# Kernel tuning notes

Hardware: AMD Instinct MI355X
Metric: run time of the kernel (lower is better)

Reference implementation:

```python
import jax, jax.numpy as jnp
import numpy as np

B, S, E, H = 4, 2048, 1024, 16
D = E // H  # head dim = 64

def setup_inputs() -> dict:
    key = jax.random.key(0)
    k1, k2, k3 = jax.random.split(key, 3)
    scale = 0.02
    return {
        "x": jax.random.normal(k1, (B, S, E), dtype=jnp.float32),
        "W_qkv": jax.random.normal(k2, (E, 3 * E), dtype=jnp.float32) * scale,
        "b_qkv": jnp.zeros((3 * E,), dtype=jnp.float32),
        "W_o": jax.random.normal(k3, (E, E), dtype=jnp.float32) * scale,
        "b_o": jnp.zeros((E,), dtype=jnp.float32),
    }

def reference(x, W_qkv, b_qkv, W_o, b_o):
    # dropout is identity in eval mode
    qkv = x @ W_qkv + b_qkv                      # [B, S, 3E]
    q, k, v = jnp.split(qkv, 3, axis=-1)          # each [B, S, E]
    def split_heads(t):
        return t.reshape(B, S, H, D).transpose(0, 2, 1, 3)  # [B, H, S, D]
    q, k, v = split_heads(q), split_heads(k), split_heads(v)
    scores = jnp.einsum("bhsd,bhtd->bhst", q, k) / jnp.sqrt(jnp.float32(D))
    causal = jnp.tril(jnp.ones((S, S), dtype=bool))
    scores = jnp.where(causal[None, None], scores, jnp.float32(-jnp.inf))
    attn = jax.nn.softmax(scores, axis=-1)        # [B, H, S, S]
    out = jnp.einsum("bhst,bhtd->bhsd", attn, v)  # [B, H, S, D]
    out = out.transpose(0, 2, 1, 3).reshape(B, S, E)
    return out @ W_o + b_o
```

## Files before the change

### kernel.cpp

```cpp
#include <hip/hip_runtime.h>
#include <stdint.h>

typedef __bf16 bf16_t;
typedef __bf16 bf16x8 __attribute__((ext_vector_type(8)));
typedef float f32x4 __attribute__((ext_vector_type(4)));

#define LOG2E 1.44269504088896340736f

__device__ __forceinline__ float fexp2(float x) {
#if __has_builtin(__builtin_amdgcn_exp2f)
    return __builtin_amdgcn_exp2f(x);
#else
    return exp2f(x);
#endif
}

__device__ __forceinline__ void gld_lds16(const bf16_t* g, bf16_t* l) {
    __builtin_amdgcn_global_load_lds(
        (__attribute__((address_space(1))) void*)(bf16_t*)g,
        (__attribute__((address_space(3))) void*)l,
        16, 0, 0);
}

__global__ __launch_bounds__(256) void prep_k(
    const float* __restrict__ x, bf16_t* __restrict__ xb,
    const float* __restrict__ Wqkv, bf16_t* __restrict__ wqkvT,
    const float* __restrict__ Wo, bf16_t* __restrict__ woT)
{
    __shared__ float t[32][33];
    const int tid = threadIdx.x;
    int blk = blockIdx.x;
    if (blk < 8192) {
        int i = blk * 1024 + tid * 4;
        float4 v = *(const float4*)(x + i);
        union { bf16_t b[4]; uint2 u; } u;
        u.b[0] = (bf16_t)v.x; u.b[1] = (bf16_t)v.y; u.b[2] = (bf16_t)v.z; u.b[3] = (bf16_t)v.w;
        *(uint2*)(xb + i) = u.u;
        return;
    }
    const float* in; bf16_t* out; int C, bx, by;
    if (blk < 11264) { blk -= 8192; in = Wqkv; out = wqkvT; C = 3072; bx = blk % 96; by = blk / 96; }
    else             { blk -= 11264; in = Wo;   out = woT;   C = 1024; bx = blk % 32; by = blk / 32; }
    const int R = 1024;
    const int tx = tid & 31, ty = tid >> 5;
    const int c0 = bx * 32, r0 = by * 32;
    #pragma unroll
    for (int j = 0; j < 32; j += 8)
        t[ty + j][tx] = in[(size_t)(r0 + ty + j) * C + c0 + tx];
    __syncthreads();
    #pragma unroll
    for (int j = 0; j < 32; j += 8)
        out[(size_t)(c0 + ty + j) * R + r0 + tx] = (bf16_t)t[tx][ty + j];
}

__device__ __forceinline__ void gemm_body_3deep(
    const bf16_t* __restrict__ A, const bf16_t* __restrict__ Bt,
    bf16_t* Al, bf16_t* Bl, f32x4 (&acc)[4][4], int m0, int n0)
{
    const int tid = threadIdx.x;
    const int w = tid >> 6, lane = tid & 63;
    const int l15 = lane & 15, quad = lane >> 4;
    const int wm = w >> 1, wn = w & 1;

    const int srow = lane >> 3;
    const int scg = ((lane & 7) ^ srow) * 8;
    const bf16_t* Ag = A  + (size_t)(m0 + w * 32 + srow) * 1024 + scg;
    const bf16_t* Bg = Bt + (size_t)(n0 + w * 16 + srow) * 1024 + scg;
    bf16_t* Ald = Al + (w * 32) * 64;
    bf16_t* Bld = Bl + (w * 16) * 64;

    const int rc0 = (quad ^ (l15 & 7)) * 8;
    const int rc1 = ((quad + 4) ^ (l15 & 7)) * 8;

    auto stage = [&](int t, int s) {
        const int koff = t * 64;
        #pragma unroll
        for (int j = 0; j < 4; j++)
            gld_lds16(Ag + koff + (size_t)(j * 8) * 1024,
                      Ald + s * 16384 + (j * 8) * 64);
        #pragma unroll
        for (int j = 0; j < 2; j++)
            gld_lds16(Bg + koff + (size_t)(j * 8) * 1024,
                      Bld + s * 8192 + (j * 8) * 64);
    };

    stage(0, 0);
    stage(1, 1);
    asm volatile("s_waitcnt vmcnt(6)" ::: "memory");
    __builtin_amdgcn_s_barrier();

    int cur = 0, stg = 2;
    for (int t = 0; t < 16; ++t) {
        if (t < 14) stage(t + 2, stg);
        const bf16_t* Ab = Al + cur * 16384;
        const bf16_t* Bb = Bl + cur * 8192;
        #pragma unroll
        for (int hh = 0; hh < 2; hh++) {
            const int rc = hh ? rc1 : rc0;
            bf16x8 af[4], bfr[4];
            #pragma unroll
            for (int mi = 0; mi < 4; mi++)
                af[mi] = *(const bf16x8*)(Ab + (wm * 64 + mi * 16 + l15) * 64 + rc);
            #pragma unroll
            for (int ni = 0; ni < 4; ni++)
                bfr[ni] = *(const bf16x8*)(Bb + (wn * 64 + ni * 16 + l15) * 64 + rc);
            __builtin_amdgcn_s_setprio(1);
            #pragma unroll
            for (int mi = 0; mi < 4; mi++)
                #pragma unroll
                for (int ni = 0; ni < 4; ni++)
                    acc[mi][ni] = __builtin_amdgcn_mfma_f32_16x16x32_bf16(
                        af[mi], bfr[ni], acc[mi][ni], 0, 0, 0);
            __builtin_amdgcn_s_setprio(0);
        }
        if (t < 15) {
            if (t < 14) asm volatile("s_waitcnt vmcnt(6)" ::: "memory");
            else        asm volatile("s_waitcnt vmcnt(0)" ::: "memory");
            __builtin_amdgcn_s_barrier();
        }
        cur = (cur == 2) ? 0 : cur + 1;
        stg = (stg == 2) ? 0 : stg + 1;
    }
}

__global__ __launch_bounds__(512) void gemm_qkv_k(
    const bf16_t* __restrict__ X, const bf16_t* __restrict__ WT,
    const float* __restrict__ bias,
    bf16_t* __restrict__ Qb, bf16_t* __restrict__ Kb, bf16_t* __restrict__ VTb)
{
    __shared__ bf16_t Al[3 * 256 * 64];
    __shared__ bf16_t Bl[3 * 128 * 64];
    const int tid = threadIdx.x;
    const int lane = tid & 63, w = tid >> 6;
    const int l15 = lane & 15, quad = lane >> 4;
    const int wm = w >> 1, wn = w & 1;
    const int n0 = blockIdx.x * 128;
    const int m0 = blockIdx.y * 256;

    f32x4 acc[4][4];
    #pragma unroll
    for (int mi = 0; mi < 4; mi++)
        #pragma unroll
        for (int ni = 0; ni < 4; ni++) acc[mi][ni] = (f32x4){0.f, 0.f, 0.f, 0.f};

    gemm_body_3deep(WT, X, Al, Bl, acc, m0, n0);

    const float QSCALE = 0.125f * LOG2E;
    const int region = m0 >> 10;
    #pragma unroll
    for (int mi = 0; mi < 4; mi++) {
        const int mbase = m0 + wm * 64 + mi * 16 + quad * 4;
        const float4 bia = *(const float4*)(bias + mbase);
        const float ba[4] = {bia.x, bia.y, bia.z, bia.w};
        const int col = mbase & 1023;
        const int h = col >> 6, dbase = col & 63;
        #pragma unroll
        for (int ni = 0; ni < 4; ni++) {
            const int n = n0 + wn * 64 + ni * 16 + l15;
            const int b = n >> 11, s = n & 2047;
            if (region == 0) {
                union { bf16_t bv[4]; uint2 u; } u;
                #pragma unroll
                for (int r = 0; r < 4; r++)
                    u.bv[r] = (bf16_t)((acc[mi][ni][r] + ba[r]) * QSCALE);
                *(uint2*)(Qb + (((size_t)b * 16 + h) * 2048 + s) * 64 + dbase) = u.u;
            } else if (region == 1) {
                union { bf16_t bv[4]; uint2 u; } u;
                #pragma unroll
                for (int r = 0; r < 4; r++)
                    u.bv[r] = (bf16_t)(acc[mi][ni][r] + ba[r]);
                *(uint2*)(Kb + (((size_t)b * 16 + h) * 2048 + s) * 64 + dbase) = u.u;
            } else {
                bf16_t* dst = VTb + (((size_t)b * 16 + h) * 64 + dbase) * 2048 + s;
                #pragma unroll
                for (int r = 0; r < 4; r++)
                    dst[(size_t)r * 2048] = (bf16_t)(acc[mi][ni][r] + ba[r]);
            }
        }
    }
}

__global__ __launch_bounds__(256) void attn_k(
    const bf16_t* __restrict__ Qb, const bf16_t* __restrict__ Kb,
    const bf16_t* __restrict__ VTb, bf16_t* __restrict__ Ob)
{
    __shared__ bf16_t Kl[64 * 64];
    __shared__ bf16_t Vl[64 * 64];
    __shared__ bf16_t Pl[4][16 * 72];

    const int tid = threadIdx.x;
    const int w = tid >> 6, lane = tid & 63;
    const int l15 = lane & 15, quad = lane >> 4;
    const int idx = blockIdx.x;
    const int qt = 31 - (idx >> 6);
    const int bh = idx & 63;
    const int b = bh >> 4, h = bh & 15;
    const int q0 = qt * 64;

    const bf16_t* Qp = Qb + (size_t)bh * 2048 * 64;
    const bf16_t* Kp = Kb + (size_t)bh * 2048 * 64;
    const bf16_t* Vp = VTb + (size_t)bh * 64 * 2048;

    const int srow = w * 16 + (lane >> 3);
    const int scol = ((lane & 7) ^ ((lane >> 3) & 7)) * 8;
    const int rc0 = (quad ^ (l15 & 7)) * 8;
    const int rc1 = ((quad + 4) ^ (l15 & 7)) * 8;

    const int qrow = q0 + w * 16 + l15;
    bf16x8 aq0 = *(const bf16x8*)(Qp + (size_t)qrow * 64 + quad * 8);
    bf16x8 aq1 = *(const bf16x8*)(Qp + (size_t)qrow * 64 + 32 + quad * 8);

    bf16x8 vone;
    #pragma unroll
    for (int j = 0; j < 8; j++) vone[j] = (bf16_t)1.0f;

    f32x4 o[4];
    #pragma unroll
    for (int ni = 0; ni < 4; ni++) o[ni] = (f32x4){0.f, 0.f, 0.f, 0.f};
    f32x4 lacc = (f32x4){0.f, 0.f, 0.f, 0.f};
    const int qloc = w * 16 + l15;

    for (int kv0 = 0; kv0 <= q0; kv0 += 64) {
        __syncthreads();
        gld_lds16(Kp + (size_t)(kv0 + srow) * 64 + scol, Kl + (w * 16) * 64);
        gld_lds16(Kp + (size_t)(kv0 + srow + 8) * 64 + scol, Kl + (w * 16 + 8) * 64);
        gld_lds16(Vp + (size_t)srow * 2048 + kv0 + scol, Vl + (w * 16) * 64);
        gld_lds16(Vp + (size_t)(srow + 8) * 2048 + kv0 + scol, Vl + (w * 16 + 8) * 64);
        __syncthreads();

        f32x4 sv[4];
        #pragma unroll
        for (int ni = 0; ni < 4; ni++) {
            bf16x8 ak0 = *(const bf16x8*)(Kl + (ni * 16 + l15) * 64 + rc0);
            bf16x8 ak1 = *(const bf16x8*)(Kl + (ni * 16 + l15) * 64 + rc1);
            f32x4 z = (f32x4){0.f, 0.f, 0.f, 0.f};
            z = __builtin_amdgcn_mfma_f32_16x16x32_bf16(ak0, aq0, z, 0, 0, 0);
            z = __builtin_amdgcn_mfma_f32_16x16x32_bf16(ak1, aq1, z, 0, 0, 0);
            sv[ni] = z;
        }

        if (kv0 == q0) {
            #pragma unroll
            for (int ni = 0; ni < 4; ni++)
                #pragma unroll
                for (int r = 0; r < 4; r++)
                    if (ni * 16 + quad * 4 + r > qloc) sv[ni][r] = -INFINITY;
        }

        #pragma unroll
        for (int ni = 0; ni < 4; ni++) {
            union { bf16_t bv[4]; uint2 u; } pk;
            #pragma unroll
            for (int r = 0; r < 4; r++) pk.bv[r] = (bf16_t)fexp2(sv[ni][r]);
            *(uint2*)(&Pl[w][l15 * 72 + ni * 16 + quad * 4]) = pk.u;
        }

        bf16x8 pa0 = *(const bf16x8*)(&Pl[w][l15 * 72 + quad * 8]);
        bf16x8 pa1 = *(const bf16x8*)(&Pl[w][l15 * 72 + 32 + quad * 8]);
        #pragma unroll
        for (int ni = 0; ni < 4; ni++) {
            bf16x8 bv0 = *(const bf16x8*)(Vl + (ni * 16 + l15) * 64 + rc0);
            bf16x8 bv1 = *(const bf16x8*)(Vl + (ni * 16 + l15) * 64 + rc1);
            o[ni] = __builtin_amdgcn_mfma_f32_16x16x32_bf16(bv0, pa0, o[ni], 0, 0, 0);
            o[ni] = __builtin_amdgcn_mfma_f32_16x16x32_bf16(bv1, pa1, o[ni], 0, 0, 0);
        }
        lacc = __builtin_amdgcn_mfma_f32_16x16x32_bf16(vone, pa0, lacc, 0, 0, 0);
        lacc = __builtin_amdgcn_mfma_f32_16x16x32_bf16(vone, pa1, lacc, 0, 0, 0);
    }

    const float inv = 1.0f / lacc[0];
    const int s = q0 + w * 16 + l15;
    bf16_t* obase = Ob + ((size_t)b * 2048 + s) * 1024 + h * 64;
    #pragma unroll
    for (int ni = 0; ni < 4; ni++) {
        union { bf16_t bv[4]; uint2 u; } u;
        #pragma unroll
        for (int r = 0; r < 4; r++) u.bv[r] = (bf16_t)(o[ni][r] * inv);
        *(uint2*)(obase + ni * 16 + quad * 4) = u.u;
    }
}

__global__ __launch_bounds__(512) void gemm_out_k(
    const bf16_t* __restrict__ O, const bf16_t* __restrict__ WT,
    const float* __restrict__ bias, float* __restrict__ out)
{
    __shared__ bf16_t Al[3 * 256 * 64];
    __shared__ bf16_t Bl[3 * 128 * 64];
    const int tid = threadIdx.x;
    const int lane = tid & 63, w = tid >> 6;
    const int l15 = lane & 15, quad = lane >> 4;
    const int wm = w >> 1, wn = w & 1;
    const int n0 = blockIdx.x * 128;
    const int m0 = blockIdx.y * 256;

    f32x4 acc[4][4];
    #pragma unroll
    for (int mi = 0; mi < 4; mi++)
        #pragma unroll
        for (int ni = 0; ni < 4; ni++) acc[mi][ni] = (f32x4){0.f, 0.f, 0.f, 0.f};

    gemm_body_3deep(WT, O, Al, Bl, acc, m0, n0);

    #pragma unroll
    for (int mi = 0; mi < 4; mi++) {
        const int mbase = m0 + wm * 64 + mi * 16 + quad * 4;
        const float4 bia = *(const float4*)(bias + mbase);
        #pragma unroll
        for (int ni = 0; ni < 4; ni++) {
            const int n = n0 + wn * 64 + ni * 16 + l15;
            float4 v;
            v.x = acc[mi][ni][0] + bia.x;
            v.y = acc[mi][ni][1] + bia.y;
            v.z = acc[mi][ni][2] + bia.z;
            v.w = acc[mi][ni][3] + bia.w;
            *(float4*)(out + (size_t)n * 1024 + mbase) = v;
        }
    }
}


extern "C" void kernel_launch(void* const* d_in, const int* in_sizes, int n_in,
                              void* d_out, int out_size, void* d_ws, size_t ws_size,
                              hipStream_t stream) {
    const float* x     = (const float*)d_in[0];
    const float* W_qkv = (const float*)d_in[1];
    const float* b_qkv = (const float*)d_in[2];
    const float* W_o   = (const float*)d_in[3];
    const float* b_o   = (const float*)d_in[4];
    float* out = (float*)d_out;

    char* ws = (char*)d_ws;
    size_t off = 0;
    auto alloc = [&](size_t bytes) -> void* {
        void* p = ws + off;
        off += (bytes + 255) & ~(size_t)255;
        return p;
    };
    bf16_t* xb    = (bf16_t*)alloc((size_t)8192 * 1024 * 2);
    bf16_t* wqkvT = (bf16_t*)alloc((size_t)3072 * 1024 * 2);
    bf16_t* woT   = (bf16_t*)alloc((size_t)1024 * 1024 * 2);
    bf16_t* Qb    = (bf16_t*)alloc((size_t)8192 * 1024 * 2);
    bf16_t* Kb    = (bf16_t*)alloc((size_t)8192 * 1024 * 2);
    bf16_t* VTb   = (bf16_t*)alloc((size_t)8192 * 1024 * 2);
    bf16_t* Ob    = xb;

    prep_k<<<12288, 256, 0, stream>>>(x, xb, W_qkv, wqkvT, W_o, woT);
    gemm_qkv_k<<<dim3(64, 12), 512, 0, stream>>>(xb, wqkvT, b_qkv, Qb, Kb, VTb);
    attn_k<<<2048, 256, 0, stream>>>(Qb, Kb, VTb, Ob);
    gemm_out_k<<<dim3(64, 4), 512, 0, stream>>>(Ob, woT, b_o, out);
}
```

Measured before the change: 255.3 us.

## Retile GEMMs to 128x256 and split global-to-LDS loads across k-halves

Both projection GEMMs flip their block tile from 256(M)x128(N) to 128(M)x256(N), with waves arranged 2x4 instead of 4x2, and the launch grids change to match. The main loop now splits each 64-wide k-tile into two halves. Each half issues part of the next-next tile's global-to-LDS loads after its LDS fragment reads, then uses barriers to separate reads from MFMAs. The aim is to spread memory traffic more evenly and overlap it with MFMA work, at the cost of four barriers per k-tile instead of one.

Measured after the change: 237.4 us. 7.0% less time.

```diff
diff --git a/kernel.cpp b/kernel.cpp
--- a/kernel.cpp
+++ b/kernel.cpp
@@ -53,57 +53,54 @@
         out[(size_t)(c0 + ty + j) * R + r0 + tx] = (bf16_t)t[tx][ty + j];
 }
 
-__device__ __forceinline__ void gemm_body_3deep(
+__device__ __forceinline__ void gemm_body_pipe(
     const bf16_t* __restrict__ A, const bf16_t* __restrict__ Bt,
     bf16_t* Al, bf16_t* Bl, f32x4 (&acc)[4][4], int m0, int n0)
 {
     const int tid = threadIdx.x;
     const int w = tid >> 6, lane = tid & 63;
     const int l15 = lane & 15, quad = lane >> 4;
-    const int wm = w >> 1, wn = w & 1;
+    const int wm = w >> 2, wn = w & 3;
 
     const int srow = lane >> 3;
     const int scg = ((lane & 7) ^ srow) * 8;
-    const bf16_t* Ag = A  + (size_t)(m0 + w * 32 + srow) * 1024 + scg;
-    const bf16_t* Bg = Bt + (size_t)(n0 + w * 16 + srow) * 1024 + scg;
-    bf16_t* Ald = Al + (w * 32) * 64;
-    bf16_t* Bld = Bl + (w * 16) * 64;
+    const bf16_t* Ag = A  + (size_t)(m0 + w * 16 + srow) * 1024 + scg;
+    const bf16_t* Bg = Bt + (size_t)(n0 + w * 32 + srow) * 1024 + scg;
 
     const int rc0 = (quad ^ (l15 & 7)) * 8;
     const int rc1 = ((quad + 4) ^ (l15 & 7)) * 8;
 
-    auto stage = [&](int t, int s) {
-        const int koff = t * 64;
-        #pragma unroll
-        for (int j = 0; j < 4; j++)
-            gld_lds16(Ag + koff + (size_t)(j * 8) * 1024,
-                      Ald + s * 16384 + (j * 8) * 64);
-        #pragma unroll
-        for (int j = 0; j < 2; j++)
-            gld_lds16(Bg + koff + (size_t)(j * 8) * 1024,
-                      Bld + s * 8192 + (j * 8) * 64);
+    auto stage0 = [&](int kt, int ss) {
+        gld_lds16(Ag + kt * 64,                       Al + ss * 8192  + (w * 16) * 64);
+        gld_lds16(Ag + kt * 64 + (size_t)8 * 1024,    Al + ss * 8192  + (w * 16 + 8) * 64);
+        gld_lds16(Bg + kt * 64,                       Bl + ss * 16384 + (w * 32) * 64);
     };
-
-    stage(0, 0);
-    stage(1, 1);
+    auto stage1 = [&](int kt, int ss) {
+        gld_lds16(Bg + kt * 64 + (size_t)8 * 1024,    Bl + ss * 16384 + (w * 32 + 8) * 64);
+        gld_lds16(Bg + kt * 64 + (size_t)16 * 1024,   Bl + ss * 16384 + (w * 32 + 16) * 64);
+        gld_lds16(Bg + kt * 64 + (size_t)24 * 1024,   Bl + ss * 16384 + (w * 32 + 24) * 64);
+    };
+
+    stage0(0, 0); stage1(0, 0);
+    stage0(1, 1); stage1(1, 1);
     asm volatile("s_waitcnt vmcnt(6)" ::: "memory");
     __builtin_amdgcn_s_barrier();
 
-    int cur = 0, stg = 2;
+    int cs = 0, ss = 2;
     for (int t = 0; t < 16; ++t) {
-        if (t < 14) stage(t + 2, stg);
-        const bf16_t* Ab = Al + cur * 16384;
-        const bf16_t* Bb = Bl + cur * 8192;
-        #pragma unroll
-        for (int hh = 0; hh < 2; hh++) {
-            const int rc = hh ? rc1 : rc0;
+        const bf16_t* Ab = Al + cs * 8192;
+        const bf16_t* Bb = Bl + cs * 16384;
+
+        {
             bf16x8 af[4], bfr[4];
             #pragma unroll
             for (int mi = 0; mi < 4; mi++)
-                af[mi] = *(const bf16x8*)(Ab + (wm * 64 + mi * 16 + l15) * 64 + rc);
+                af[mi] = *(const bf16x8*)(Ab + (wm * 64 + mi * 16 + l15) * 64 + rc0);
             #pragma unroll
             for (int ni = 0; ni < 4; ni++)
-                bfr[ni] = *(const bf16x8*)(Bb + (wn * 64 + ni * 16 + l15) * 64 + rc);
+                bfr[ni] = *(const bf16x8*)(Bb + (wn * 64 + ni * 16 + l15) * 64 + rc0);
+            if (t < 14) stage0(t + 2, ss);
+            __builtin_amdgcn_s_barrier();
             __builtin_amdgcn_s_setprio(1);
             #pragma unroll
             for (int mi = 0; mi < 4; mi++)
@@ -112,14 +109,37 @@
                     acc[mi][ni] = __builtin_amdgcn_mfma_f32_16x16x32_bf16(
                         af[mi], bfr[ni], acc[mi][ni], 0, 0, 0);
             __builtin_amdgcn_s_setprio(0);
-        }
-        if (t < 15) {
-            if (t < 14) asm volatile("s_waitcnt vmcnt(6)" ::: "memory");
-            else        asm volatile("s_waitcnt vmcnt(0)" ::: "memory");
             __builtin_amdgcn_s_barrier();
         }
-        cur = (cur == 2) ? 0 : cur + 1;
-        stg = (stg == 2) ? 0 : stg + 1;
+
+        {
+            bf16x8 af[4], bfr[4];
+            #pragma unroll
+            for (int mi = 0; mi < 4; mi++)
+                af[mi] = *(const bf16x8*)(Ab + (wm * 64 + mi * 16 + l15) * 64 + rc1);
+            #pragma unroll
+            for (int ni = 0; ni < 4; ni++)
+                bfr[ni] = *(const bf16x8*)(Bb + (wn * 64 + ni * 16 + l15) * 64 + rc1);
+            if (t < 14) {
+                stage1(t + 2, ss);
+                asm volatile("s_waitcnt vmcnt(6)" ::: "memory");
+            } else if (t == 14) {
+                asm volatile("s_waitcnt vmcnt(0)" ::: "memory");
+            }
+            __builtin_amdgcn_s_barrier();
+            __builtin_amdgcn_s_setprio(1);
+            #pragma unroll
+            for (int mi = 0; mi < 4; mi++)
+                #pragma unroll
+                for (int ni = 0; ni < 4; ni++)
+                    acc[mi][ni] = __builtin_amdgcn_mfma_f32_16x16x32_bf16(
+                        af[mi], bfr[ni], acc[mi][ni], 0, 0, 0);
+            __builtin_amdgcn_s_setprio(0);
+            __builtin_amdgcn_s_barrier();
+        }
+
+        cs = (cs == 2) ? 0 : cs + 1;
+        ss = (ss == 2) ? 0 : ss + 1;
     }
 }
 
@@ -128,14 +148,14 @@
     const float* __restrict__ bias,
     bf16_t* __restrict__ Qb, bf16_t* __restrict__ Kb, bf16_t* __restrict__ VTb)
 {
-    __shared__ bf16_t Al[3 * 256 * 64];
-    __shared__ bf16_t Bl[3 * 128 * 64];
+    __shared__ bf16_t Al[3 * 128 * 64];
+    __shared__ bf16_t Bl[3 * 256 * 64];
     const int tid = threadIdx.x;
     const int lane = tid & 63, w = tid >> 6;
     const int l15 = lane & 15, quad = lane >> 4;
-    const int wm = w >> 1, wn = w & 1;
-    const int n0 = blockIdx.x * 128;
-    const int m0 = blockIdx.y * 256;
+    const int wm = w >> 2, wn = w & 3;
+    const int n0 = blockIdx.x * 256;
+    const int m0 = blockIdx.y * 128;
 
     f32x4 acc[4][4];
     #pragma unroll
@@ -143,7 +163,7 @@
         #pragma unroll
         for (int ni = 0; ni < 4; ni++) acc[mi][ni] = (f32x4){0.f, 0.f, 0.f, 0.f};
 
-    gemm_body_3deep(WT, X, Al, Bl, acc, m0, n0);
+    gemm_body_pipe(WT, X, Al, Bl, acc, m0, n0);
 
     const float QSCALE = 0.125f * LOG2E;
     const int region = m0 >> 10;
@@ -284,14 +304,14 @@
     const bf16_t* __restrict__ O, const bf16_t* __restrict__ WT,
     const float* __restrict__ bias, float* __restrict__ out)
 {
-    __shared__ bf16_t Al[3 * 256 * 64];
-    __shared__ bf16_t Bl[3 * 128 * 64];
+    __shared__ bf16_t Al[3 * 128 * 64];
+    __shared__ bf16_t Bl[3 * 256 * 64];
     const int tid = threadIdx.x;
     const int lane = tid & 63, w = tid >> 6;
     const int l15 = lane & 15, quad = lane >> 4;
-    const int wm = w >> 1, wn = w & 1;
-    const int n0 = blockIdx.x * 128;
-    const int m0 = blockIdx.y * 256;
+    const int wm = w >> 2, wn = w & 3;
+    const int n0 = blockIdx.x * 256;
+    const int m0 = blockIdx.y * 128;
 
     f32x4 acc[4][4];
     #pragma unroll
@@ -299,7 +319,7 @@
         #pragma unroll
         for (int ni = 0; ni < 4; ni++) acc[mi][ni] = (f32x4){0.f, 0.f, 0.f, 0.f};
 
-    gemm_body_3deep(WT, O, Al, Bl, acc, m0, n0);
+    gemm_body_pipe(WT, O, Al, Bl, acc, m0, n0);
 
     #pragma unroll
     for (int mi = 0; mi < 4; mi++) {
@@ -345,7 +365,7 @@
     bf16_t* Ob    = xb;
 
     prep_k<<<12288, 256, 0, stream>>>(x, xb, W_qkv, wqkvT, W_o, woT);
-    gemm_qkv_k<<<dim3(64, 12), 512, 0, stream>>>(xb, wqkvT, b_qkv, Qb, Kb, VTb);
+    gemm_qkv_k<<<dim3(32, 24), 512, 0, stream>>>(xb, wqkvT, b_qkv, Qb, Kb, VTb);
     attn_k<<<2048, 256, 0, stream>>>(Qb, Kb, VTb, Ob);
-    gemm_out_k<<<dim3(64, 4), 512, 0, stream>>>(Ob, woT, b_o, out);
-}
+    gemm_out_k<<<dim3(32, 8), 512, 0, stream>>>(Ob, woT, b_o, out);
+}
```
